# Optimization experiments

Measured on AMD Instinct MI355X. Metric: run time of the kernel, lower is better.

Reference implementation:

```python
import jax, jax.numpy as jnp
import numpy as np

N = 20000          # nodes
E = 320000         # edges (avg degree 16)
HID = 256          # hidden_size
HEADS = 8          # num_heads
HD = HID // HEADS  # head_dim = 32


def setup_inputs() -> dict:
    key = jax.random.key(0)
    ks = jax.random.split(key, 12)
    scale = 1.0 / np.sqrt(HID).astype(np.float32)
    def lin_w(k):
        return jax.random.normal(k, (HID, HID), jnp.float32) * scale
    def lin_b(k):
        return jax.random.normal(k, (HID,), jnp.float32) * 0.01
    return {
        "h":   jax.random.normal(ks[0], (N, HID), jnp.float32),
        "Wq": lin_w(ks[1]), "bq": lin_b(ks[2]),
        "Wk": lin_w(ks[3]), "bk": lin_b(ks[4]),
        "Wv": lin_w(ks[5]), "bv": lin_b(ks[6]),
        "Wo": lin_w(ks[7]), "bo": lin_b(ks[8]),
        "rows": jax.random.randint(ks[9],  (E,), 0, N),  # dst/query node of each edge
        "cols": jax.random.randint(ks[10], (E,), 0, N),  # src/key node of each edge
    }


def reference(h, Wq, bq, Wk, bk, Wv, bv, Wo, bo, rows, cols):
    n = h.shape[0]
    scaling = HD ** (-0.5)
    # projections; reshape exactly as torch: (N, head_dim, num_heads)
    q = ((h @ Wq) + bq).reshape(n, HD, HEADS) * scaling
    k = ((h @ Wk) + bk).reshape(n, HD, HEADS)
    v = ((h @ Wv) + bv).reshape(n, HD, HEADS)
    # bsddmm: per-edge, per-head score s[e,h] = sum_d q[rows[e],d,h] * k[cols[e],d,h]
    s = jnp.einsum("edh,edh->eh", q[rows], k[cols])  # [E, HEADS]
    # sparse row-wise softmax (over each row's edges)
    m = jax.ops.segment_max(s, rows, num_segments=n)          # [N, HEADS]
    e = jnp.exp(s - m[rows])                                   # [E, HEADS]
    z = jax.ops.segment_sum(e, rows, num_segments=n)           # [N, HEADS]
    attn = e / z[rows]                                          # [E, HEADS]
    # bspmm: out[i,d,h] = sum_{e: rows[e]=i} attn[e,h] * v[cols[e],d,h]
    out = jax.ops.segment_sum(attn[:, None, :] * v[cols], rows, num_segments=n)  # [N, HD, HEADS]
    return out.reshape(n, -1) @ Wo + bo
```

## Files before the change

### kernel.cpp

```cpp
#include <hip/hip_runtime.h>
#include <hip/hip_bf16.h>
#include <math.h>

#define NNODES 20000
#define NEDGES 320000

using f32x4 = __attribute__((ext_vector_type(4))) float;
using s16x8 = __attribute__((ext_vector_type(8))) short;
using u16x8 = __attribute__((ext_vector_type(8))) unsigned short;

__device__ __forceinline__ float bf2f(unsigned short u) {
    union { unsigned int i; float f; } c; c.i = ((unsigned int)u) << 16; return c.f;
}
__device__ __forceinline__ unsigned short f2bf(float f) {
    __hip_bfloat16 h = __float2bfloat16(f);
    return *reinterpret_cast<unsigned short*>(&h);
}

__global__ __launch_bounds__(256) void prep_k(
    const float* __restrict__ Wq, const float* __restrict__ bq,
    const float* __restrict__ Wk, const float* __restrict__ bk,
    const float* __restrict__ Wv, const float* __restrict__ bv,
    const float* __restrict__ Wo,
    unsigned short* __restrict__ wt, float* __restrict__ bp)
{
    const int gid = blockIdx.x * 256 + threadIdx.x;
    const float SC = 0.17677669529663687f;
    if (gid < 262144) {
        const int mat = gid >> 16, r = gid & 65535;
        if (mat < 3) {
            const int k = r >> 8, c = r & 255;
            const int n_old = ((c & 31) << 3) | (c >> 5);
            const float* W = (mat == 0) ? Wq : (mat == 1) ? Wk : Wv;
            float val = W[k * 256 + n_old];
            if (mat == 0) val *= SC;
            wt[mat * 65536 + c * 256 + k] = f2bf(val);
        } else {
            const int c = r >> 8, n = r & 255;
            const int n_old = ((c & 31) << 3) | (c >> 5);
            wt[3 * 65536 + n * 256 + c] = f2bf(Wo[n_old * 256 + n]);
        }
    } else if (gid < 262912) {
        const int idx = gid - 262144;
        const int mat = idx >> 8, c = idx & 255;
        const int n_old = ((c & 31) << 3) | (c >> 5);
        const float* b = (mat == 0) ? bq : (mat == 1) ? bk : bv;
        float val = b[n_old];
        if (mat == 0) val *= SC;
        bp[mat * 256 + c] = val;
    }
}

__global__ __launch_bounds__(256) void hcvt_k(const float* __restrict__ h,
                                              unsigned short* __restrict__ hb)
{
    const int i = (blockIdx.x * 256 + threadIdx.x) * 4;
    const float4 f = *reinterpret_cast<const float4*>(&h[i]);
    ushort4 u;
    u.x = f2bf(f.x); u.y = f2bf(f.y); u.z = f2bf(f.z); u.w = f2bf(f.w);
    *reinterpret_cast<ushort4*>(&hb[i]) = u;
}

__global__ __launch_bounds__(256) void qkv_mfma_k(
    const unsigned short* __restrict__ hb,
    const unsigned short* __restrict__ wt, const float* __restrict__ bp,
    unsigned short* __restrict__ qo, unsigned short* __restrict__ ko,
    unsigned short* __restrict__ vo)
{
    const int bm = blockIdx.x * 128;
    const int mat = blockIdx.y >> 1;
    const int bn = (blockIdx.y & 1) * 128;
    unsigned short* outp = (mat == 0) ? qo : (mat == 1) ? ko : vo;
    const unsigned short* W = wt + mat * 65536;
    const float* bias = bp + mat * 256;

    __shared__ __align__(16) unsigned short As[128][40];
    __shared__ __align__(16) unsigned short Bs[128][40];

    const int t = threadIdx.x;
    const int lane = t & 63, w = t >> 6;
    const int wr = (w >> 1) * 64, wc = (w & 1) * 64;

    f32x4 acc[4][4];
    #pragma unroll
    for (int i = 0; i < 4; ++i)
        #pragma unroll
        for (int j = 0; j < 4; ++j) acc[i][j] = (f32x4){0.f, 0.f, 0.f, 0.f};

    const int srow = t >> 2, koff = (t & 3) * 8;
    for (int kt = 0; kt < 8; ++kt) {
        const int k0 = kt * 32;
        const int m0 = min(bm + srow, NNODES - 1);
        const int m1 = min(bm + srow + 64, NNODES - 1);
        *reinterpret_cast<u16x8*>(&As[srow][koff]) =
            *reinterpret_cast<const u16x8*>(&hb[m0 * 256 + k0 + koff]);
        *reinterpret_cast<u16x8*>(&As[srow + 64][koff]) =
            *reinterpret_cast<const u16x8*>(&hb[m1 * 256 + k0 + koff]);
        *reinterpret_cast<u16x8*>(&Bs[srow][koff]) =
            *reinterpret_cast<const u16x8*>(&W[(bn + srow) * 256 + k0 + koff]);
        *reinterpret_cast<u16x8*>(&Bs[srow + 64][koff]) =
            *reinterpret_cast<const u16x8*>(&W[(bn + srow + 64) * 256 + k0 + koff]);
        __syncthreads();
        s16x8 a[4], b[4];
        const int kk = (lane >> 4) * 8;
        #pragma unroll
        for (int i = 0; i < 4; ++i) {
            a[i] = *reinterpret_cast<const s16x8*>(&As[wr + i * 16 + (lane & 15)][kk]);
            b[i] = *reinterpret_cast<const s16x8*>(&Bs[wc + i * 16 + (lane & 15)][kk]);
        }
        #pragma unroll
        for (int i = 0; i < 4; ++i)
            #pragma unroll
            for (int j = 0; j < 4; ++j)
                acc[i][j] = __builtin_amdgcn_mfma_f32_16x16x32_bf16(a[i], b[j], acc[i][j], 0, 0, 0);
        __syncthreads();
    }
    #pragma unroll
    for (int i = 0; i < 4; ++i)
        #pragma unroll
        for (int j = 0; j < 4; ++j) {
            const int n = bn + wc + j * 16 + (lane & 15);
            const float bval = bias[n];
            #pragma unroll
            for (int r = 0; r < 4; ++r) {
                const int m = bm + wr + i * 16 + (lane >> 4) * 4 + r;
                if (m < NNODES) outp[m * 256 + n] = f2bf(acc[i][j][r] + bval);
            }
        }
}

__global__ __launch_bounds__(256) void out_mfma_k(
    const unsigned short* __restrict__ A,
    const unsigned short* __restrict__ wt, const float* __restrict__ bo,
    float* __restrict__ C)
{
    const int bm = blockIdx.x * 128;
    const int bn = blockIdx.y * 128;
    const unsigned short* W = wt + 3 * 65536;

    __shared__ __align__(16) unsigned short As[128][40];
    __shared__ __align__(16) unsigned short Bs[128][40];

    const int t = threadIdx.x;
    const int lane = t & 63, w = t >> 6;
    const int wr = (w >> 1) * 64, wc = (w & 1) * 64;

    f32x4 acc[4][4];
    #pragma unroll
    for (int i = 0; i < 4; ++i)
        #pragma unroll
        for (int j = 0; j < 4; ++j) acc[i][j] = (f32x4){0.f, 0.f, 0.f, 0.f};

    const int srow = t >> 2, koff = (t & 3) * 8;
    for (int kt = 0; kt < 8; ++kt) {
        const int k0 = kt * 32;
        const int m0 = min(bm + srow, NNODES - 1);
        const int m1 = min(bm + srow + 64, NNODES - 1);
        *reinterpret_cast<u16x8*>(&As[srow][koff]) =
            *reinterpret_cast<const u16x8*>(&A[m0 * 256 + k0 + koff]);
        *reinterpret_cast<u16x8*>(&As[srow + 64][koff]) =
            *reinterpret_cast<const u16x8*>(&A[m1 * 256 + k0 + koff]);
        *reinterpret_cast<u16x8*>(&Bs[srow][koff]) =
            *reinterpret_cast<const u16x8*>(&W[(bn + srow) * 256 + k0 + koff]);
        *reinterpret_cast<u16x8*>(&Bs[srow + 64][koff]) =
            *reinterpret_cast<const u16x8*>(&W[(bn + srow + 64) * 256 + k0 + koff]);
        __syncthreads();
        s16x8 a[4], b[4];
        const int kk = (lane >> 4) * 8;
        #pragma unroll
        for (int i = 0; i < 4; ++i) {
            a[i] = *reinterpret_cast<const s16x8*>(&As[wr + i * 16 + (lane & 15)][kk]);
            b[i] = *reinterpret_cast<const s16x8*>(&Bs[wc + i * 16 + (lane & 15)][kk]);
        }
        #pragma unroll
        for (int i = 0; i < 4; ++i)
            #pragma unroll
            for (int j = 0; j < 4; ++j)
                acc[i][j] = __builtin_amdgcn_mfma_f32_16x16x32_bf16(a[i], b[j], acc[i][j], 0, 0, 0);
        __syncthreads();
    }
    #pragma unroll
    for (int i = 0; i < 4; ++i)
        #pragma unroll
        for (int j = 0; j < 4; ++j) {
            const int n = bn + wc + j * 16 + (lane & 15);
            const float bval = bo[n];
            #pragma unroll
            for (int r = 0; r < 4; ++r) {
                const int m = bm + wr + i * 16 + (lane >> 4) * 4 + r;
                if (m < NNODES) C[m * 256 + n] = acc[i][j][r] + bval;
            }
        }
}

__global__ void hist_k(const int* __restrict__ rows, int* __restrict__ counts)
{
    const int i = blockIdx.x * blockDim.x + threadIdx.x;
    if (i < NEDGES) atomicAdd(&counts[rows[i]], 1);
}

__global__ __launch_bounds__(256) void scan_k(const int* __restrict__ counts,
                                              int* __restrict__ row_start)
{
    __shared__ int wsum[4];
    __shared__ int s_carry;
    const int t = threadIdx.x, lane = t & 63, w = t >> 6;
    if (t == 0) { s_carry = 0; row_start[0] = 0; }
    __syncthreads();
    for (int base = 0; base < NNODES; base += 1024) {
        int c[4]; int s4 = 0;
        #pragma unroll
        for (int j = 0; j < 4; ++j) {
            const int idx = base + t * 4 + j;
            c[j] = (idx < NNODES) ? counts[idx] : 0;
            s4 += c[j];
        }
        int incl = s4;
        #pragma unroll
        for (int off = 1; off < 64; off <<= 1) {
            const int y = __shfl_up(incl, off);
            if (lane >= off) incl += y;
        }
        if (lane == 63) wsum[w] = incl;
        __syncthreads();
        int prev = 0;
        for (int i = 0; i < w; ++i) prev += wsum[i];
        const int total = wsum[0] + wsum[1] + wsum[2] + wsum[3];
        int run = s_carry + prev + incl - s4;
        #pragma unroll
        for (int j = 0; j < 4; ++j) {
            const int idx = base + t * 4 + j;
            run += c[j];
            if (idx < NNODES) row_start[idx + 1] = run;
        }
        __syncthreads();
        if (t == 0) s_carry += total;
        __syncthreads();
    }
}

__global__ void scatter_k(const int* __restrict__ rows, const int* __restrict__ cols,
                          const int* __restrict__ row_start, int* __restrict__ cursor,
                          int* __restrict__ cols_sorted)
{
    const int i = blockIdx.x * blockDim.x + threadIdx.x;
    if (i < NEDGES) {
        const int r = rows[i];
        const int pos = row_start[r] + atomicAdd(&cursor[r], 1);
        cols_sorted[pos] = cols[i];
    }
}

__global__ __launch_bounds__(256) void row_attn_k(
    const unsigned short* __restrict__ q, const unsigned short* __restrict__ k,
    const unsigned short* __restrict__ v,
    const int* __restrict__ row_start, const int* __restrict__ cols_sorted,
    unsigned short* __restrict__ ot)
{
    const int lane = threadIdx.x & 63;
    const int row = blockIdx.x * 4 + (threadIdx.x >> 6);
    if (row >= NNODES) return;
    const int rs = row_start[row], re = row_start[row + 1];
    const int col4 = lane * 4;

    const ushort4 qu = *reinterpret_cast<const ushort4*>(&q[row * 256 + col4]);
    const float q0 = bf2f(qu.x), q1 = bf2f(qu.y), q2 = bf2f(qu.z), q3 = bf2f(qu.w);
    float z = 0.f, o0 = 0.f, o1 = 0.f, o2 = 0.f, o3 = 0.f;

    for (int c0 = rs; c0 < re; c0 += 64) {
        const int nch = min(64, re - c0);
        const int cn_reg = (c0 + lane < re) ? cols_sorted[c0 + lane] : 0;
        #pragma unroll 2
        for (int i = 0; i < nch; ++i) {
            const int cn = __shfl(cn_reg, i);
            const ushort4 ku = *reinterpret_cast<const ushort4*>(&k[cn * 256 + col4]);
            const ushort4 vu = *reinterpret_cast<const ushort4*>(&v[cn * 256 + col4]);
            float p = q0 * bf2f(ku.x);
            p = fmaf(q1, bf2f(ku.y), p);
            p = fmaf(q2, bf2f(ku.z), p);
            p = fmaf(q3, bf2f(ku.w), p);
            p += __shfl_xor(p, 1);
            p += __shfl_xor(p, 2);
            p += __shfl_xor(p, 4);
            const float e = __expf(p);
            z += e;
            o0 = fmaf(e, bf2f(vu.x), o0);
            o1 = fmaf(e, bf2f(vu.y), o1);
            o2 = fmaf(e, bf2f(vu.z), o2);
            o3 = fmaf(e, bf2f(vu.w), o3);
        }
    }
    ushort4 r;
    if (re > rs) {
        const float iz = 1.0f / z;
        r.x = f2bf(o0 * iz); r.y = f2bf(o1 * iz);
        r.z = f2bf(o2 * iz); r.w = f2bf(o3 * iz);
    } else {
        r.x = r.y = r.z = r.w = 0;
    }
    *reinterpret_cast<ushort4*>(&ot[row * 256 + col4]) = r;
}

extern "C" void kernel_launch(void* const* d_in, const int* in_sizes, int n_in,
                              void* d_out, int out_size, void* d_ws, size_t ws_size,
                              hipStream_t stream)
{
    const float* h  = (const float*)d_in[0];
    const float* Wq = (const float*)d_in[1];
    const float* bq = (const float*)d_in[2];
    const float* Wk = (const float*)d_in[3];
    const float* bk = (const float*)d_in[4];
    const float* Wv = (const float*)d_in[5];
    const float* bv = (const float*)d_in[6];
    const float* Wo = (const float*)d_in[7];
    const float* bo = (const float*)d_in[8];
    const int* rows = (const int*)d_in[9];
    const int* cols = (const int*)d_in[10];
    float* outp = (float*)d_out;

    char* ws = (char*)d_ws;
    unsigned short* q_b  = (unsigned short*)(ws + 0);
    unsigned short* k_b  = (unsigned short*)(ws + 10240000);
    unsigned short* v_b  = (unsigned short*)(ws + 20480000);
    unsigned short* ot_b = (unsigned short*)(ws + 30720000);
    unsigned short* h_b  = (unsigned short*)(ws + 40960000);
    unsigned short* wt   = (unsigned short*)(ws + 51200000);
    float* bp            = (float*)(ws + 51724288);
    int* row_start       = (int*)(ws + 51727360);
    int* counts          = (int*)(ws + 51807488);
    int* cursor          = (int*)(ws + 51887488);
    int* cols_sorted     = (int*)(ws + 51967488);

    hipMemsetAsync(ws + 51807488, 0, 160000, stream);

    prep_k<<<1027, 256, 0, stream>>>(Wq, bq, Wk, bk, Wv, bv, Wo, wt, bp);
    hcvt_k<<<5000, 256, 0, stream>>>(h, h_b);
    hist_k<<<1250, 256, 0, stream>>>(rows, counts);
    scan_k<<<1, 256, 0, stream>>>(counts, row_start);
    scatter_k<<<1250, 256, 0, stream>>>(rows, cols, row_start, cursor, cols_sorted);
    qkv_mfma_k<<<dim3(157, 6), 256, 0, stream>>>(h_b, wt, bp, q_b, k_b, v_b);
    row_attn_k<<<5000, 256, 0, stream>>>(q_b, k_b, v_b, row_start, cols_sorted, ot_b);
    out_mfma_k<<<dim3(157, 2), 256, 0, stream>>>(ot_b, wt, bo, outp);
}
```

Measured before the change: 242.4 us.

## Interleave K/V per node, fuse h conversion into QKV GEMM and merge prep kernels

K and V are stored interleaved in a single [N,512] buffer, so the attention kernel fetches each neighbour's K and V slice with one 16-byte load instead of two 8-byte loads. The separate h-to-bf16 conversion kernel is removed and the QKV GEMM now reads fp32 h directly and converts it while staging into shared memory. The histogram is folded into the weight-prep kernel, the scan runs with 1024 threads, and the attention inner loop unroll goes from 2 to 4. The trade-offs are more global reads in the GEMM, since it loads fp32 h once per output tile, and scattered 2-byte stores in the GEMM epilogue.

```diff
diff --git a/kernel.cpp b/kernel.cpp
--- a/kernel.cpp
+++ b/kernel.cpp
@@ -17,12 +17,13 @@
     return *reinterpret_cast<unsigned short*>(&h);
 }
 
-__global__ __launch_bounds__(256) void prep_k(
+__global__ __launch_bounds__(256) void prep_hist_k(
     const float* __restrict__ Wq, const float* __restrict__ bq,
     const float* __restrict__ Wk, const float* __restrict__ bk,
     const float* __restrict__ Wv, const float* __restrict__ bv,
-    const float* __restrict__ Wo,
-    unsigned short* __restrict__ wt, float* __restrict__ bp)
+    const float* __restrict__ Wo, const int* __restrict__ rows,
+    unsigned short* __restrict__ wt, float* __restrict__ bp,
+    int* __restrict__ counts)
 {
     const int gid = blockIdx.x * 256 + threadIdx.x;
     const float SC = 0.17677669529663687f;
@@ -48,29 +49,73 @@
         float val = b[n_old];
         if (mat == 0) val *= SC;
         bp[mat * 256 + c] = val;
-    }
-}
-
-__global__ __launch_bounds__(256) void hcvt_k(const float* __restrict__ h,
-                                              unsigned short* __restrict__ hb)
-{
-    const int i = (blockIdx.x * 256 + threadIdx.x) * 4;
-    const float4 f = *reinterpret_cast<const float4*>(&h[i]);
-    ushort4 u;
-    u.x = f2bf(f.x); u.y = f2bf(f.y); u.z = f2bf(f.z); u.w = f2bf(f.w);
-    *reinterpret_cast<ushort4*>(&hb[i]) = u;
+    } else if (gid < 262912 + NEDGES) {
+        atomicAdd(&counts[rows[gid - 262912]], 1);
+    }
+}
+
+__global__ __launch_bounds__(1024) void scan_k(const int* __restrict__ counts,
+                                               int* __restrict__ row_start)
+{
+    __shared__ int wsum[16];
+    __shared__ int s_carry;
+    const int t = threadIdx.x, lane = t & 63, w = t >> 6;
+    if (t == 0) { s_carry = 0; row_start[0] = 0; }
+    __syncthreads();
+    for (int base = 0; base < NNODES; base += 4096) {
+        int c[4]; int s4 = 0;
+        #pragma unroll
+        for (int j = 0; j < 4; ++j) {
+            const int idx = base + t * 4 + j;
+            c[j] = (idx < NNODES) ? counts[idx] : 0;
+            s4 += c[j];
+        }
+        int incl = s4;
+        #pragma unroll
+        for (int off = 1; off < 64; off <<= 1) {
+            const int y = __shfl_up(incl, off);
+            if (lane >= off) incl += y;
+        }
+        if (lane == 63) wsum[w] = incl;
+        __syncthreads();
+        int prev = 0;
+        for (int i = 0; i < w; ++i) prev += wsum[i];
+        int total = 0;
+        #pragma unroll
+        for (int i = 0; i < 16; ++i) total += wsum[i];
+        int run = s_carry + prev + incl - s4;
+        #pragma unroll
+        for (int j = 0; j < 4; ++j) {
+            const int idx = base + t * 4 + j;
+            run += c[j];
+            if (idx < NNODES) row_start[idx + 1] = run;
+        }
+        __syncthreads();
+        if (t == 0) s_carry += total;
+        __syncthreads();
+    }
+}
+
+__global__ void scatter_k(const int* __restrict__ rows, const int* __restrict__ cols,
+                          const int* __restrict__ row_start, int* __restrict__ cursor,
+                          int* __restrict__ cols_sorted)
+{
+    const int i = blockIdx.x * blockDim.x + threadIdx.x;
+    if (i < NEDGES) {
+        const int r = rows[i];
+        const int pos = row_start[r] + atomicAdd(&cursor[r], 1);
+        cols_sorted[pos] = cols[i];
+    }
 }
 
 __global__ __launch_bounds__(256) void qkv_mfma_k(
-    const unsigned short* __restrict__ hb,
+    const float* __restrict__ h,
     const unsigned short* __restrict__ wt, const float* __restrict__ bp,
-    unsigned short* __restrict__ qo, unsigned short* __restrict__ ko,
-    unsigned short* __restrict__ vo)
+    unsigned short* __restrict__ qo, unsigned short* __restrict__ kv)
 {
     const int bm = blockIdx.x * 128;
     const int mat = blockIdx.y >> 1;
     const int bn = (blockIdx.y & 1) * 128;
-    unsigned short* outp = (mat == 0) ? qo : (mat == 1) ? ko : vo;
     const unsigned short* W = wt + mat * 65536;
     const float* bias = bp + mat * 256;
 
@@ -92,10 +137,20 @@
         const int k0 = kt * 32;
         const int m0 = min(bm + srow, NNODES - 1);
         const int m1 = min(bm + srow + 64, NNODES - 1);
-        *reinterpret_cast<u16x8*>(&As[srow][koff]) =
-            *reinterpret_cast<const u16x8*>(&hb[m0 * 256 + k0 + koff]);
-        *reinterpret_cast<u16x8*>(&As[srow + 64][koff]) =
-            *reinterpret_cast<const u16x8*>(&hb[m1 * 256 + k0 + koff]);
+        {
+            const float4 fa = *reinterpret_cast<const float4*>(&h[m0 * 256 + k0 + koff]);
+            const float4 fb = *reinterpret_cast<const float4*>(&h[m0 * 256 + k0 + koff + 4]);
+            u16x8 u; u[0]=f2bf(fa.x); u[1]=f2bf(fa.y); u[2]=f2bf(fa.z); u[3]=f2bf(fa.w);
+                     u[4]=f2bf(fb.x); u[5]=f2bf(fb.y); u[6]=f2bf(fb.z); u[7]=f2bf(fb.w);
+            *reinterpret_cast<u16x8*>(&As[srow][koff]) = u;
+        }
+        {
+            const float4 fa = *reinterpret_cast<const float4*>(&h[m1 * 256 + k0 + koff]);
+            const float4 fb = *reinterpret_cast<const float4*>(&h[m1 * 256 + k0 + koff + 4]);
+            u16x8 u; u[0]=f2bf(fa.x); u[1]=f2bf(fa.y); u[2]=f2bf(fa.z); u[3]=f2bf(fa.w);
+                     u[4]=f2bf(fb.x); u[5]=f2bf(fb.y); u[6]=f2bf(fb.z); u[7]=f2bf(fb.w);
+            *reinterpret_cast<u16x8*>(&As[srow + 64][koff]) = u;
+        }
         *reinterpret_cast<u16x8*>(&Bs[srow][koff]) =
             *reinterpret_cast<const u16x8*>(&W[(bn + srow) * 256 + k0 + koff]);
         *reinterpret_cast<u16x8*>(&Bs[srow + 64][koff]) =
@@ -121,10 +176,15 @@
         for (int j = 0; j < 4; ++j) {
             const int n = bn + wc + j * 16 + (lane & 15);
             const float bval = bias[n];
+            const int kvbase = ((n >> 2) << 3) + (n & 3) + ((mat == 2) ? 4 : 0);
             #pragma unroll
             for (int r = 0; r < 4; ++r) {
                 const int m = bm + wr + i * 16 + (lane >> 4) * 4 + r;
-                if (m < NNODES) outp[m * 256 + n] = f2bf(acc[i][j][r] + bval);
+                if (m < NNODES) {
+                    const unsigned short val = f2bf(acc[i][j][r] + bval);
+                    if (mat == 0) qo[m * 256 + n] = val;
+                    else          kv[m * 512 + kvbase] = val;
+                }
             }
         }
 }
@@ -193,67 +253,8 @@
         }
 }
 
-__global__ void hist_k(const int* __restrict__ rows, int* __restrict__ counts)
-{
-    const int i = blockIdx.x * blockDim.x + threadIdx.x;
-    if (i < NEDGES) atomicAdd(&counts[rows[i]], 1);
-}
-
-__global__ __launch_bounds__(256) void scan_k(const int* __restrict__ counts,
-                                              int* __restrict__ row_start)
-{
-    __shared__ int wsum[4];
-    __shared__ int s_carry;
-    const int t = threadIdx.x, lane = t & 63, w = t >> 6;
-    if (t == 0) { s_carry = 0; row_start[0] = 0; }
-    __syncthreads();
-    for (int base = 0; base < NNODES; base += 1024) {
-        int c[4]; int s4 = 0;
-        #pragma unroll
-        for (int j = 0; j < 4; ++j) {
-            const int idx = base + t * 4 + j;
-            c[j] = (idx < NNODES) ? counts[idx] : 0;
-            s4 += c[j];
-        }
-        int incl = s4;
-        #pragma unroll
-        for (int off = 1; off < 64; off <<= 1) {
-            const int y = __shfl_up(incl, off);
-            if (lane >= off) incl += y;
-        }
-        if (lane == 63) wsum[w] = incl;
-        __syncthreads();
-        int prev = 0;
-        for (int i = 0; i < w; ++i) prev += wsum[i];
-        const int total = wsum[0] + wsum[1] + wsum[2] + wsum[3];
-        int run = s_carry + prev + incl - s4;
-        #pragma unroll
-        for (int j = 0; j < 4; ++j) {
-            const int idx = base + t * 4 + j;
-            run += c[j];
-            if (idx < NNODES) row_start[idx + 1] = run;
-        }
-        __syncthreads();
-        if (t == 0) s_carry += total;
-        __syncthreads();
-    }
-}
-
-__global__ void scatter_k(const int* __restrict__ rows, const int* __restrict__ cols,
-                          const int* __restrict__ row_start, int* __restrict__ cursor,
-                          int* __restrict__ cols_sorted)
-{
-    const int i = blockIdx.x * blockDim.x + threadIdx.x;
-    if (i < NEDGES) {
-        const int r = rows[i];
-        const int pos = row_start[r] + atomicAdd(&cursor[r], 1);
-        cols_sorted[pos] = cols[i];
-    }
-}
-
 __global__ __launch_bounds__(256) void row_attn_k(
-    const unsigned short* __restrict__ q, const unsigned short* __restrict__ k,
-    const unsigned short* __restrict__ v,
+    const unsigned short* __restrict__ q, const unsigned short* __restrict__ kv,
     const int* __restrict__ row_start, const int* __restrict__ cols_sorted,
     unsigned short* __restrict__ ot)
 {
@@ -261,33 +262,31 @@
     const int row = blockIdx.x * 4 + (threadIdx.x >> 6);
     if (row >= NNODES) return;
     const int rs = row_start[row], re = row_start[row + 1];
-    const int col4 = lane * 4;
-
-    const ushort4 qu = *reinterpret_cast<const ushort4*>(&q[row * 256 + col4]);
+
+    const ushort4 qu = *reinterpret_cast<const ushort4*>(&q[row * 256 + lane * 4]);
     const float q0 = bf2f(qu.x), q1 = bf2f(qu.y), q2 = bf2f(qu.z), q3 = bf2f(qu.w);
     float z = 0.f, o0 = 0.f, o1 = 0.f, o2 = 0.f, o3 = 0.f;
 
     for (int c0 = rs; c0 < re; c0 += 64) {
         const int nch = min(64, re - c0);
         const int cn_reg = (c0 + lane < re) ? cols_sorted[c0 + lane] : 0;
-        #pragma unroll 2
+        #pragma unroll 4
         for (int i = 0; i < nch; ++i) {
             const int cn = __shfl(cn_reg, i);
-            const ushort4 ku = *reinterpret_cast<const ushort4*>(&k[cn * 256 + col4]);
-            const ushort4 vu = *reinterpret_cast<const ushort4*>(&v[cn * 256 + col4]);
-            float p = q0 * bf2f(ku.x);
-            p = fmaf(q1, bf2f(ku.y), p);
-            p = fmaf(q2, bf2f(ku.z), p);
-            p = fmaf(q3, bf2f(ku.w), p);
+            const u16x8 kv8 = *reinterpret_cast<const u16x8*>(&kv[cn * 512 + lane * 8]);
+            float p = q0 * bf2f(kv8[0]);
+            p = fmaf(q1, bf2f(kv8[1]), p);
+            p = fmaf(q2, bf2f(kv8[2]), p);
+            p = fmaf(q3, bf2f(kv8[3]), p);
             p += __shfl_xor(p, 1);
             p += __shfl_xor(p, 2);
             p += __shfl_xor(p, 4);
             const float e = __expf(p);
             z += e;
-            o0 = fmaf(e, bf2f(vu.x), o0);
-            o1 = fmaf(e, bf2f(vu.y), o1);
-            o2 = fmaf(e, bf2f(vu.z), o2);
-            o3 = fmaf(e, bf2f(vu.w), o3);
+            o0 = fmaf(e, bf2f(kv8[4]), o0);
+            o1 = fmaf(e, bf2f(kv8[5]), o1);
+            o2 = fmaf(e, bf2f(kv8[6]), o2);
+            o3 = fmaf(e, bf2f(kv8[7]), o3);
         }
     }
     ushort4 r;
@@ -298,7 +297,7 @@
     } else {
         r.x = r.y = r.z = r.w = 0;
     }
-    *reinterpret_cast<ushort4*>(&ot[row * 256 + col4]) = r;
+    *reinterpret_cast<ushort4*>(&ot[row * 256 + lane * 4]) = r;
 }
 
 extern "C" void kernel_launch(void* const* d_in, const int* in_sizes, int n_in,
@@ -320,25 +319,22 @@
 
     char* ws = (char*)d_ws;
     unsigned short* q_b  = (unsigned short*)(ws + 0);
-    unsigned short* k_b  = (unsigned short*)(ws + 10240000);
-    unsigned short* v_b  = (unsigned short*)(ws + 20480000);
+    unsigned short* kv_b = (unsigned short*)(ws + 10240000);
     unsigned short* ot_b = (unsigned short*)(ws + 30720000);
-    unsigned short* h_b  = (unsigned short*)(ws + 40960000);
-    unsigned short* wt   = (unsigned short*)(ws + 51200000);
-    float* bp            = (float*)(ws + 51724288);
-    int* row_start       = (int*)(ws + 51727360);
-    int* counts          = (int*)(ws + 51807488);
-    int* cursor          = (int*)(ws + 51887488);
-    int* cols_sorted     = (int*)(ws + 51967488);
-
-    hipMemsetAsync(ws + 51807488, 0, 160000, stream);
-
-    prep_k<<<1027, 256, 0, stream>>>(Wq, bq, Wk, bk, Wv, bv, Wo, wt, bp);
-    hcvt_k<<<5000, 256, 0, stream>>>(h, h_b);
-    hist_k<<<1250, 256, 0, stream>>>(rows, counts);
-    scan_k<<<1, 256, 0, stream>>>(counts, row_start);
+    unsigned short* wt   = (unsigned short*)(ws + 40960000);
+    float* bp            = (float*)(ws + 41484288);
+    int* row_start       = (int*)(ws + 41487360);
+    int* counts          = (int*)(ws + 41567488);
+    int* cursor          = (int*)(ws + 41647488);
+    int* cols_sorted     = (int*)(ws + 41727488);
+
+    hipMemsetAsync(ws + 41567488, 0, 160000, stream);
+
+    prep_hist_k<<<2277, 256, 0, stream>>>(Wq, bq, Wk, bk, Wv, bv, Wo, rows,
+                                          wt, bp, counts);
+    scan_k<<<1, 1024, 0, stream>>>(counts, row_start);
     scatter_k<<<1250, 256, 0, stream>>>(rows, cols, row_start, cursor, cols_sorted);
-    qkv_mfma_k<<<dim3(157, 6), 256, 0, stream>>>(h_b, wt, bp, q_b, k_b, v_b);
-    row_attn_k<<<5000, 256, 0, stream>>>(q_b, k_b, v_b, row_start, cols_sorted, ot_b);
+    qkv_mfma_k<<<dim3(157, 6), 256, 0, stream>>>(h, wt, bp, q_b, kv_b);
+    row_attn_k<<<5000, 256, 0, stream>>>(q_b, kv_b, row_start, cols_sorted, ot_b);
     out_mfma_k<<<dim3(157, 2), 256, 0, stream>>>(ot_b, wt, bo, outp);
 }
```

New measurement: 231.8 us. -4.4%, faster.
